# Optimization experiments

Measured on AMD Instinct MI355X. Metric: run time of the kernel, lower is better.

## Reference

```python
import jax, jax.numpy as jnp
import numpy as np

LN_EPS = 1e-9
NEG_INF = float(-2**32 + 1)


def setup_inputs() -> dict:
    key = jax.random.key(0)
    k1, k2 = jax.random.split(key)
    B, T, C = 64, 1024, 256
    x = jax.random.normal(k1, (B, T, C), dtype=jnp.float32)
    key_masks = jax.random.randint(k2, (B, 1, T), 0, 2) > 0  # bool [B,1,T]
    gamma = jnp.ones((C,), dtype=jnp.float32)
    beta = jnp.zeros((C,), dtype=jnp.float32)
    return {"x": x, "key_masks": key_masks, "gamma": gamma, "beta": beta}


def reference(x, key_masks, gamma, beta):
    # x: [B,T,C]; key_masks: [B,1,T] bool; gamma/beta: [C]
    B, T, C = x.shape
    inv_scale = 1.0 / np.sqrt(C).astype(np.float32)
    # DotAttention: QK^T scaled -> [B,T,T]
    align = jnp.einsum('btc,bsc->bts', x, x) * inv_scale
    # key padding mask (broadcast over query axis)
    align = jnp.where(key_masks, align, NEG_INF)
    # future binding: causal lower-triangular mask
    causal = jnp.tril(jnp.ones((T, T), dtype=bool))
    align = jnp.where(causal[None, :, :], align, NEG_INF)
    attn = jax.nn.softmax(align, axis=-1)  # dropout_rate=0 / inference -> identity
    out = jnp.einsum('bts,bsc->btc', attn, x)  # [B,T,C]
    # LayerNorm over last axis
    mu = jnp.mean(out, axis=-1, keepdims=True)
    var = jnp.mean(jnp.square(out - mu), axis=-1, keepdims=True)
    out = gamma * (out - mu) * jax.lax.rsqrt(var + LN_EPS) + beta
    # reduce_mean over time axis, keepdims
    return jnp.mean(out, axis=1, keepdims=True)  # [B,1,C]
```

## Files before the change

kernel.cpp:

```cpp
#include <hip/hip_runtime.h>

#define B_   64
#define T_   1024
#define C_   256
#define NEGF (-4294967295.0f)
#define LN_EPS 1e-9f

typedef short  short8 __attribute__((ext_vector_type(8)));
typedef float  f32x4  __attribute__((ext_vector_type(4)));

union S8 { short8 v; unsigned int w[4]; };

__device__ __forceinline__ unsigned int pk2(float x, float y) {
  unsigned a = __float_as_uint(x); a = (a + 0x7fffu + ((a >> 16) & 1u)) >> 16;
  unsigned b = __float_as_uint(y); b = (b + 0x7fffu + ((b >> 16) & 1u)) >> 16;
  return a | (b << 16);
}

__device__ __forceinline__ void async16(const void* g, void* l) {
  __builtin_amdgcn_global_load_lds(
      (const __attribute__((address_space(1))) void*)g,
      (__attribute__((address_space(3))) void*)l,
      16, 0, 0);
}


__global__ void detect_kernel(const unsigned int* __restrict__ mw,
                              int* __restrict__ flag) {
  int idx = blockIdx.x * 256 + threadIdx.x;
  if (mw[idx] > 1u) atomicOr(flag, 1);
}

__global__ void finalize_kernel(const float* __restrict__ accum,
                                float* __restrict__ out) {
  int idx = blockIdx.x * 256 + threadIdx.x;
  out[idx] = accum[idx] * (1.0f / T_);
}

__global__ __launch_bounds__(256) void convert_kv(const float* __restrict__ x,
                                                  const unsigned int* __restrict__ mw,
                                                  const int* __restrict__ flag,
                                                  short* __restrict__ xk,
                                                  short* __restrict__ xv,
                                                  float* __restrict__ colsum,
                                                  float2* __restrict__ sb) {
  __shared__ float Xt[32 * 256];
  const int blk = blockIdx.x, b = blk >> 5, tt = blk & 31;
  const int tid = threadIdx.x;
  const float* xt = x + (size_t)(b * 1024 + tt * 32) * 256;

  if (tid < 32) {
    int idx = b * 1024 + tt * 32 + tid;
    int f = *flag;
    unsigned int w = mw[f ? (idx >> 2) : idx];
    unsigned int v = f ? ((w >> ((idx & 3) * 8)) & 0xffu) : w;
    sb[idx] = v ? make_float2(0.0625f, 0.f) : make_float2(0.f, NEGF);
  }

#pragma unroll
  for (int u = 0; u < 4; ++u) {
    int id = u * 256 + tid;
    int row = id >> 5, ck = id & 31;
    const float* src = xt + row * 256 + ck * 8;
    float4 a  = *(const float4*)src;
    float4 c4 = *(const float4*)(src + 4);
    *(float4*)&Xt[row * 256 + ck * 8]     = a;
    *(float4*)&Xt[row * 256 + ck * 8 + 4] = c4;
    S8 s; s.w[0] = pk2(a.x, a.y);  s.w[1] = pk2(a.z, a.w);
          s.w[2] = pk2(c4.x, c4.y); s.w[3] = pk2(c4.z, c4.w);
    *(short8*)(xk + (size_t)(b * 1024 + tt * 32 + row) * 256 + ((ck ^ row) << 3)) = s.v;
  }
  __syncthreads();

  const int ck = tid >> 6, clo = tid & 63;
  short* vout = xv + (size_t)(b * 32 + tt) * 8192;
#pragma unroll
  for (int g = 0; g < 4; ++g) {
    int c = g * 64 + clo;
    float vs[8]; float s = 0.f;
#pragma unroll
    for (int e = 0; e < 8; ++e) { vs[e] = Xt[(ck * 8 + e) * 256 + c]; s += vs[e]; }
    S8 o;
    o.w[0] = pk2(vs[0], vs[1]); o.w[1] = pk2(vs[2], vs[3]);
    o.w[2] = pk2(vs[4], vs[5]); o.w[3] = pk2(vs[6], vs[7]);
    *(short8*)(vout + c * 32 + (((ck ^ ((c >> 1) & 3)) & 3) << 3)) = o.v;
    atomicAdd(&colsum[b * 256 + c], s);
  }
}

__device__ __forceinline__ void finalize_tile(
    f32x4* Oa, float m, float l, int b, int quad, int r,
    const float* __restrict__ colsum, const float* __restrict__ gamma,
    const float* __restrict__ beta, float* __restrict__ accum)
{
  float mr[4], li[4];
#pragma unroll
  for (int reg = 0; reg < 4; ++reg) {
    mr[reg] = __shfl(m, quad * 4 + reg, 64);
    float lr = __shfl(l, quad * 4 + reg, 64);
    li[reg] = 1.f / lr;
  }
#pragma unroll
  for (int ct = 0; ct < 16; ++ct) {
    float cs = colsum[b * C_ + ct * 16 + r] * (1.0f / T_);
#pragma unroll
    for (int reg = 0; reg < 4; ++reg)
      Oa[ct][reg] = (mr[reg] < -1.0e9f) ? cs : Oa[ct][reg] * li[reg];
  }
  float ts[16];
#pragma unroll
  for (int ct = 0; ct < 16; ++ct) ts[ct] = 0.f;
#pragma unroll
  for (int reg = 0; reg < 4; ++reg) {
    float s2 = 0.f;
#pragma unroll
    for (int ct = 0; ct < 16; ++ct) s2 += Oa[ct][reg];
    s2 += __shfl_xor(s2, 1, 64); s2 += __shfl_xor(s2, 2, 64);
    s2 += __shfl_xor(s2, 4, 64); s2 += __shfl_xor(s2, 8, 64);
    float mu = s2 * (1.0f / C_);
    float sq = 0.f;
#pragma unroll
    for (int ct = 0; ct < 16; ++ct) { float d = Oa[ct][reg] - mu; sq += d * d; }
    sq += __shfl_xor(sq, 1, 64); sq += __shfl_xor(sq, 2, 64);
    sq += __shfl_xor(sq, 4, 64); sq += __shfl_xor(sq, 8, 64);
    float rstd = rsqrtf(sq * (1.0f / C_) + LN_EPS);
#pragma unroll
    for (int ct = 0; ct < 16; ++ct) {
      int c = ct * 16 + r;
      ts[ct] += gamma[c] * (Oa[ct][reg] - mu) * rstd + beta[c];
    }
  }
#pragma unroll
  for (int ct = 0; ct < 16; ++ct) {
    ts[ct] += __shfl_xor(ts[ct], 16, 64);
    ts[ct] += __shfl_xor(ts[ct], 32, 64);
  }
  if (quad == 0) {
#pragma unroll
    for (int ct = 0; ct < 16; ++ct)
      atomicAdd(&accum[b * C_ + ct * 16 + r], ts[ct]);
  }
}

__global__ __launch_bounds__(512, 2) void flash5(
    const short* __restrict__ xk,
    const short* __restrict__ xv,
    const float2* __restrict__ sb,
    const float* __restrict__ gamma,
    const float* __restrict__ beta,
    const float* __restrict__ colsum,
    float* __restrict__ accum)
{
  __shared__ __align__(16) short KsD[2][64 * 256];
  __shared__ __align__(16) short VtD[2][2 * 256 * 32];

  const int i0 = blockIdx.x;
  const int x8 = i0 & 7;
  const int s  = i0 >> 3;
  const int b  = x8 + 8 * (s & 7);
  const int t  = s >> 3;

  const int tid  = threadIdx.x;
  const int w    = tid >> 6;
  const int lane = tid & 63;
  const int quad = lane >> 4;
  const int r    = lane & 15;

  const int h0len = 2 * (t + 1);

  int qt   = t;
  int n0   = qt * 128 + w * 16;
  int qrow = n0 + r;
  short8 qf[8];
  {
    const short* qp = xk + (size_t)(b * 1024 + qrow) * 256;
#pragma unroll
    for (int ks = 0; ks < 8; ++ks)
      qf[ks] = *(const short8*)(qp + (((ks * 4 + quad) ^ (qrow & 31)) << 3));
  }
  f32x4 Oa[16];
#pragma unroll
  for (int ct = 0; ct < 16; ++ct) Oa[ct] = (f32x4){0.f, 0.f, 0.f, 0.f};
  float m = NEGF, l = 0.f;

  {
    const short* gk = xk + (size_t)(b * 1024) * 256;
    const short* gv = xv + (size_t)(b * 32) * 8192;
#pragma unroll
    for (int u = 0; u < 4; ++u) {
      int seg = w * 4 + u;
      async16(gk + seg * 512 + lane * 8, &KsD[0][seg * 512]);
      async16(gv + seg * 512 + lane * 8, &VtD[0][seg * 512]);
    }
  }
  __syncthreads();

  for (int idx = 0; idx < 18; ++idx) {
    const int ibuf = idx & 1;
    if (idx < 17) {
      const int nt2 = (idx + 1 < h0len) ? (idx + 1) : (17 - (idx + 1));
      const short* gk = xk + (size_t)(b * 1024 + nt2 * 64) * 256;
      const short* gv = xv + (size_t)(b * 32 + nt2 * 2) * 8192;
#pragma unroll
      for (int u = 0; u < 4; ++u) {
        int seg = w * 4 + u;
        async16(gk + seg * 512 + lane * 8, &KsD[1 - ibuf][seg * 512]);
        async16(gv + seg * 512 + lane * 8, &VtD[1 - ibuf][seg * 512]);
      }
    }

    const int kt  = (idx < h0len) ? idx : (17 - idx);
    const int ktb = kt * 64;
    if (ktb <= n0 + 15) {
      float sc[16];
#pragma unroll
      for (int mt = 0; mt < 4; ++mt) {
        f32x4 acc = (f32x4){0.f, 0.f, 0.f, 0.f};
        const int row = mt * 16 + r;
#pragma unroll
        for (int ks = 0; ks < 8; ++ks) {
          short8 af = *(short8*)&KsD[ibuf][row * 256 + (((ks * 4 + quad) ^ (row & 31)) << 3)];
          acc = __builtin_amdgcn_mfma_f32_16x16x32_bf16(af, qf[ks], acc, 0, 0, 0);
        }
        const int j0 = ktb + mt * 16 + quad * 4;
        float4 sA = *(const float4*)(sb + (size_t)b * 1024 + j0);
        float4 sB = *(const float4*)(sb + (size_t)b * 1024 + j0 + 2);
        sc[mt * 4 + 0] = acc[0] * sA.x + sA.y;
        sc[mt * 4 + 1] = acc[1] * sA.z + sA.w;
        sc[mt * 4 + 2] = acc[2] * sB.x + sB.y;
        sc[mt * 4 + 3] = acc[3] * sB.z + sB.w;
      }
      if (ktb + 63 > n0) {
#pragma unroll
        for (int k2 = 0; k2 < 16; ++k2) {
          int j = ktb + (k2 >> 2) * 16 + quad * 4 + (k2 & 3);
          if (j > qrow) sc[k2] = NEGF;
        }
      }

      float mx = sc[0];
#pragma unroll
      for (int k2 = 1; k2 < 16; ++k2) mx = fmaxf(mx, sc[k2]);
      mx = fmaxf(mx, __shfl_xor(mx, 16, 64));
      mx = fmaxf(mx, __shfl_xor(mx, 32, 64));
      float mnew  = fmaxf(m, mx);
      float alpha = __expf(m - mnew);
      float p[16], ps = 0.f;
#pragma unroll
      for (int k2 = 0; k2 < 16; ++k2) { p[k2] = __expf(sc[k2] - mnew); ps += p[k2]; }
      ps += __shfl_xor(ps, 16, 64);
      ps += __shfl_xor(ps, 32, 64);
      l = l * alpha + ps;
      m = mnew;

      if (__ballot(alpha < 1.0f)) {
        float ar[4];
#pragma unroll
        for (int reg = 0; reg < 4; ++reg) ar[reg] = __shfl(alpha, quad * 4 + reg, 64);
#pragma unroll
        for (int ct = 0; ct < 16; ++ct) {
          Oa[ct][0] *= ar[0]; Oa[ct][1] *= ar[1];
          Oa[ct][2] *= ar[2]; Oa[ct][3] *= ar[3];
        }
      }

      S8 pf[2];
#pragma unroll
      for (int hh = 0; hh < 2; ++hh) {
        unsigned q0 = pk2(p[hh * 8 + 0], p[hh * 8 + 1]);
        unsigned q1 = pk2(p[hh * 8 + 2], p[hh * 8 + 3]);
        unsigned q2 = pk2(p[hh * 8 + 4], p[hh * 8 + 5]);
        unsigned q3 = pk2(p[hh * 8 + 6], p[hh * 8 + 7]);
        int s0l = ((quad & 1) << 5) + r, s1l = s0l + 16;
        unsigned u0 = __shfl((int)q0, s0l, 64), u1 = __shfl((int)q1, s0l, 64);
        unsigned u2 = __shfl((int)q2, s0l, 64), u3 = __shfl((int)q3, s0l, 64);
        unsigned v0 = __shfl((int)q0, s1l, 64), v1 = __shfl((int)q1, s1l, 64);
        unsigned v2 = __shfl((int)q2, s1l, 64), v3 = __shfl((int)q3, s1l, 64);
        bool hi = quad >= 2;
        pf[hh].w[0] = hi ? u2 : u0; pf[hh].w[1] = hi ? u3 : u1;
        pf[hh].w[2] = hi ? v2 : v0; pf[hh].w[3] = hi ? v3 : v1;
      }

#pragma unroll
      for (int ct = 0; ct < 16; ++ct) {
        int c = ct * 16 + r;
        int cs_off = c * 32 + (((quad ^ ((c >> 1) & 3)) & 3) << 3);
        short8 b0 = *(short8*)&VtD[ibuf][cs_off];
        short8 b1 = *(short8*)&VtD[ibuf][8192 + cs_off];
        Oa[ct] = __builtin_amdgcn_mfma_f32_16x16x32_bf16(pf[0].v, b0, Oa[ct], 0, 0, 0);
        Oa[ct] = __builtin_amdgcn_mfma_f32_16x16x32_bf16(pf[1].v, b1, Oa[ct], 0, 0, 0);
      }
    }

    if (idx == h0len - 1) {
      finalize_tile(Oa, m, l, b, quad, r, colsum, gamma, beta, accum);
      qt = 7 - t;
      n0 = qt * 128 + w * 16;
      qrow = n0 + r;
      const short* qp = xk + (size_t)(b * 1024 + qrow) * 256;
#pragma unroll
      for (int ks = 0; ks < 8; ++ks)
        qf[ks] = *(const short8*)(qp + (((ks * 4 + quad) ^ (qrow & 31)) << 3));
#pragma unroll
      for (int ct = 0; ct < 16; ++ct) Oa[ct] = (f32x4){0.f, 0.f, 0.f, 0.f};
      m = NEGF; l = 0.f;
    }

    __syncthreads();
  }

  finalize_tile(Oa, m, l, b, quad, r, colsum, gamma, beta, accum);
}


extern "C" void kernel_launch(void* const* d_in, const int* in_sizes, int n_in,
                              void* d_out, int out_size, void* d_ws, size_t ws_size,
                              hipStream_t stream) {
  const float* x     = (const float*)d_in[0];
  const void*  km    = d_in[1];
  const float* gamma = (const float*)d_in[2];
  const float* beta  = (const float*)d_in[3];
  float* out = (float*)d_out;

  const size_t off_sb = 131200;
  const size_t off_xk = 655616;
  const size_t off_xv = off_xk + 33554432;

  float*  accum  = (float*)d_ws;
  float*  colsum = (float*)((char*)d_ws + 65536);
  int*    flag   = (int*)((char*)d_ws + 131072);
  float2* sb     = (float2*)((char*)d_ws + off_sb);
  short*  xk     = (short*)((char*)d_ws + off_xk);
  short*  xv     = (short*)((char*)d_ws + off_xv);

  hipMemsetAsync(d_ws, 0, 131136, stream);
  detect_kernel<<<64, 256, 0, stream>>>((const unsigned int*)km, flag);
  convert_kv<<<B_ * 32, 256, 0, stream>>>(x, (const unsigned int*)km, flag,
                                          xk, xv, colsum, sb);
  flash5<<<256, 512, 0, stream>>>(xk, xv, sb, gamma, beta, colsum, accum);
  finalize_kernel<<<B_ * C_ / 256, 256, 0, stream>>>(accum, out);
}
```

Measured before the change: 181.4 us.

## Restructure flash kernel to 4-wave blocks with two query tiles per wave

```diff
diff --git a/kernel.cpp b/kernel.cpp
--- a/kernel.cpp
+++ b/kernel.cpp
@@ -5,6 +5,7 @@
 #define C_   256
 #define NEGF (-4294967295.0f)
 #define LN_EPS 1e-9f
+#define XTS  260
 
 typedef short  short8 __attribute__((ext_vector_type(8)));
 typedef float  f32x4  __attribute__((ext_vector_type(4)));
@@ -44,10 +45,13 @@
                                                   short* __restrict__ xv,
                                                   float* __restrict__ colsum,
                                                   float2* __restrict__ sb) {
-  __shared__ float Xt[32 * 256];
+  __shared__ float Xt[32 * XTS];
+  __shared__ float csum[256];
   const int blk = blockIdx.x, b = blk >> 5, tt = blk & 31;
   const int tid = threadIdx.x;
   const float* xt = x + (size_t)(b * 1024 + tt * 32) * 256;
+
+  csum[tid] = 0.f;
 
   if (tid < 32) {
     int idx = b * 1024 + tt * 32 + tid;
@@ -64,8 +68,8 @@
     const float* src = xt + row * 256 + ck * 8;
     float4 a  = *(const float4*)src;
     float4 c4 = *(const float4*)(src + 4);
-    *(float4*)&Xt[row * 256 + ck * 8]     = a;
-    *(float4*)&Xt[row * 256 + ck * 8 + 4] = c4;
+    *(float4*)&Xt[row * XTS + ck * 8]     = a;
+    *(float4*)&Xt[row * XTS + ck * 8 + 4] = c4;
     S8 s; s.w[0] = pk2(a.x, a.y);  s.w[1] = pk2(a.z, a.w);
           s.w[2] = pk2(c4.x, c4.y); s.w[3] = pk2(c4.z, c4.w);
     *(short8*)(xk + (size_t)(b * 1024 + tt * 32 + row) * 256 + ((ck ^ row) << 3)) = s.v;
@@ -79,13 +83,56 @@
     int c = g * 64 + clo;
     float vs[8]; float s = 0.f;
 #pragma unroll
-    for (int e = 0; e < 8; ++e) { vs[e] = Xt[(ck * 8 + e) * 256 + c]; s += vs[e]; }
+    for (int e = 0; e < 8; ++e) { vs[e] = Xt[(ck * 8 + e) * XTS + c]; s += vs[e]; }
     S8 o;
     o.w[0] = pk2(vs[0], vs[1]); o.w[1] = pk2(vs[2], vs[3]);
     o.w[2] = pk2(vs[4], vs[5]); o.w[3] = pk2(vs[6], vs[7]);
     *(short8*)(vout + c * 32 + (((ck ^ ((c >> 1) & 3)) & 3) << 3)) = o.v;
-    atomicAdd(&colsum[b * 256 + c], s);
-  }
+    atomicAdd(&csum[c], s);
+  }
+  __syncthreads();
+  atomicAdd(&colsum[b * 256 + tid], csum[tid]);
+}
+
+
+__device__ __forceinline__ S8 softmax_step(const float* sc, float& m, float& l,
+                                           f32x4* Oa, int quad, int r) {
+  float mx = sc[0];
+#pragma unroll
+  for (int k2 = 1; k2 < 8; ++k2) mx = fmaxf(mx, sc[k2]);
+  mx = fmaxf(mx, __shfl_xor(mx, 16, 64));
+  mx = fmaxf(mx, __shfl_xor(mx, 32, 64));
+  float mnew  = fmaxf(m, mx);
+  float alpha = __expf(m - mnew);
+  float p[8], ps = 0.f;
+#pragma unroll
+  for (int k2 = 0; k2 < 8; ++k2) { p[k2] = __expf(sc[k2] - mnew); ps += p[k2]; }
+  ps += __shfl_xor(ps, 16, 64);
+  ps += __shfl_xor(ps, 32, 64);
+  l = l * alpha + ps;
+  m = mnew;
+  if (__ballot(alpha < 1.0f)) {
+    float ar[4];
+#pragma unroll
+    for (int reg = 0; reg < 4; ++reg) ar[reg] = __shfl(alpha, quad * 4 + reg, 64);
+#pragma unroll
+    for (int ct = 0; ct < 16; ++ct) {
+      Oa[ct][0] *= ar[0]; Oa[ct][1] *= ar[1];
+      Oa[ct][2] *= ar[2]; Oa[ct][3] *= ar[3];
+    }
+  }
+  unsigned q0 = pk2(p[0], p[1]), q1 = pk2(p[2], p[3]);
+  unsigned q2 = pk2(p[4], p[5]), q3 = pk2(p[6], p[7]);
+  int s0l = ((quad & 1) << 5) + r, s1l = s0l + 16;
+  unsigned u0 = __shfl((int)q0, s0l, 64), u1 = __shfl((int)q1, s0l, 64);
+  unsigned u2 = __shfl((int)q2, s0l, 64), u3 = __shfl((int)q3, s0l, 64);
+  unsigned v0 = __shfl((int)q0, s1l, 64), v1 = __shfl((int)q1, s1l, 64);
+  unsigned v2 = __shfl((int)q2, s1l, 64), v3 = __shfl((int)q3, s1l, 64);
+  bool hi = quad >= 2;
+  S8 pf;
+  pf.w[0] = hi ? u2 : u0; pf.w[1] = hi ? u3 : u1;
+  pf.w[2] = hi ? v2 : v0; pf.w[3] = hi ? v3 : v1;
+  return pf;
 }
 
 __device__ __forceinline__ void finalize_tile(
@@ -142,7 +189,7 @@
   }
 }
 
-__global__ __launch_bounds__(512, 2) void flash5(
+__global__ __launch_bounds__(256, 2) void flash7(
     const short* __restrict__ xk,
     const short* __restrict__ xv,
     const float2* __restrict__ sb,
@@ -151,14 +198,18 @@
     const float* __restrict__ colsum,
     float* __restrict__ accum)
 {
-  __shared__ __align__(16) short KsD[2][64 * 256];
-  __shared__ __align__(16) short VtD[2][2 * 256 * 32];
-
-  const int i0 = blockIdx.x;
-  const int x8 = i0 & 7;
-  const int s  = i0 >> 3;
-  const int b  = x8 + 8 * (s & 7);
-  const int t  = s >> 3;
+  __shared__ __align__(16) short KsD[2][32 * 256];
+  __shared__ __align__(16) short VtD[2][256 * 32];
+
+  const int i0   = blockIdx.x;
+  const int half = i0 >> 8;
+  const int j    = i0 & 255;
+  const int x8   = j & 7;
+  const int v    = j >> 3;
+  const int b    = x8 + 8 * (v & 7);
+  const int tc   = v >> 3;
+  const int tau  = half ? tc : (7 - tc);
+  const int niters = 4 * tau + 4;
 
   const int tid  = threadIdx.x;
   const int w    = tid >> 6;
@@ -166,22 +217,28 @@
   const int quad = lane >> 4;
   const int r    = lane & 15;
 
-  const int h0len = 2 * (t + 1);
-
-  int qt   = t;
-  int n0   = qt * 128 + w * 16;
-  int qrow = n0 + r;
-  short8 qf[8];
+  const int n0a = tau * 128 + w * 16;
+  const int n0b = n0a + 64;
+  const int qrowA = n0a + r, qrowB = n0b + r;
+
+  short8 qfA[8], qfB[8];
   {
-    const short* qp = xk + (size_t)(b * 1024 + qrow) * 256;
-#pragma unroll
-    for (int ks = 0; ks < 8; ++ks)
-      qf[ks] = *(const short8*)(qp + (((ks * 4 + quad) ^ (qrow & 31)) << 3));
-  }
-  f32x4 Oa[16];
-#pragma unroll
-  for (int ct = 0; ct < 16; ++ct) Oa[ct] = (f32x4){0.f, 0.f, 0.f, 0.f};
-  float m = NEGF, l = 0.f;
+    const short* qa = xk + (size_t)(b * 1024 + qrowA) * 256;
+    const short* qb = xk + (size_t)(b * 1024 + qrowB) * 256;
+#pragma unroll
+    for (int ks = 0; ks < 8; ++ks) {
+      qfA[ks] = *(const short8*)(qa + (((ks * 4 + quad) ^ (qrowA & 31)) << 3));
+      qfB[ks] = *(const short8*)(qb + (((ks * 4 + quad) ^ (qrowB & 31)) << 3));
+    }
+  }
+
+  f32x4 OaA[16], OaB[16];
+#pragma unroll
+  for (int ct = 0; ct < 16; ++ct) {
+    OaA[ct] = (f32x4){0.f, 0.f, 0.f, 0.f};
+    OaB[ct] = (f32x4){0.f, 0.f, 0.f, 0.f};
+  }
+  float mA = NEGF, lA = 0.f, mB = NEGF, lB = 0.f;
 
   {
     const short* gk = xk + (size_t)(b * 1024) * 256;
@@ -195,12 +252,11 @@
   }
   __syncthreads();
 
-  for (int idx = 0; idx < 18; ++idx) {
-    const int ibuf = idx & 1;
-    if (idx < 17) {
-      const int nt2 = (idx + 1 < h0len) ? (idx + 1) : (17 - (idx + 1));
-      const short* gk = xk + (size_t)(b * 1024 + nt2 * 64) * 256;
-      const short* gv = xv + (size_t)(b * 32 + nt2 * 2) * 8192;
+  for (int kt = 0; kt < niters; ++kt) {
+    const int ibuf = kt & 1;
+    if (kt + 1 < niters) {
+      const short* gk = xk + (size_t)(b * 1024 + (kt + 1) * 32) * 256;
+      const short* gv = xv + (size_t)(b * 32 + (kt + 1)) * 8192;
 #pragma unroll
       for (int u = 0; u < 4; ++u) {
         int seg = w * 4 + u;
@@ -209,107 +265,76 @@
       }
     }
 
-    const int kt  = (idx < h0len) ? idx : (17 - idx);
-    const int ktb = kt * 64;
-    if (ktb <= n0 + 15) {
-      float sc[16];
-#pragma unroll
-      for (int mt = 0; mt < 4; ++mt) {
-        f32x4 acc = (f32x4){0.f, 0.f, 0.f, 0.f};
+    const int ktb = kt * 32;
+    const bool bAct = (ktb <= n0b + 15);
+    const bool aAct = (ktb <= n0a + 15);
+    if (bAct) {
+      float scA[8], scB[8];
+#pragma unroll
+      for (int mt = 0; mt < 2; ++mt) {
+        f32x4 aA = (f32x4){0.f, 0.f, 0.f, 0.f};
+        f32x4 aB = (f32x4){0.f, 0.f, 0.f, 0.f};
         const int row = mt * 16 + r;
 #pragma unroll
         for (int ks = 0; ks < 8; ++ks) {
-          short8 af = *(short8*)&KsD[ibuf][row * 256 + (((ks * 4 + quad) ^ (row & 31)) << 3)];
-          acc = __builtin_amdgcn_mfma_f32_16x16x32_bf16(af, qf[ks], acc, 0, 0, 0);
+          short8 af = *(short8*)&KsD[ibuf][row * 256 + (((ks * 4 + quad) ^ row) << 3)];
+          aB = __builtin_amdgcn_mfma_f32_16x16x32_bf16(af, qfB[ks], aB, 0, 0, 0);
+          if (aAct)
+            aA = __builtin_amdgcn_mfma_f32_16x16x32_bf16(af, qfA[ks], aA, 0, 0, 0);
         }
         const int j0 = ktb + mt * 16 + quad * 4;
-        float4 sA = *(const float4*)(sb + (size_t)b * 1024 + j0);
-        float4 sB = *(const float4*)(sb + (size_t)b * 1024 + j0 + 2);
-        sc[mt * 4 + 0] = acc[0] * sA.x + sA.y;
-        sc[mt * 4 + 1] = acc[1] * sA.z + sA.w;
-        sc[mt * 4 + 2] = acc[2] * sB.x + sB.y;
-        sc[mt * 4 + 3] = acc[3] * sB.z + sB.w;
-      }
-      if (ktb + 63 > n0) {
-#pragma unroll
-        for (int k2 = 0; k2 < 16; ++k2) {
-          int j = ktb + (k2 >> 2) * 16 + quad * 4 + (k2 & 3);
-          if (j > qrow) sc[k2] = NEGF;
-        }
-      }
-
-      float mx = sc[0];
-#pragma unroll
-      for (int k2 = 1; k2 < 16; ++k2) mx = fmaxf(mx, sc[k2]);
-      mx = fmaxf(mx, __shfl_xor(mx, 16, 64));
-      mx = fmaxf(mx, __shfl_xor(mx, 32, 64));
-      float mnew  = fmaxf(m, mx);
-      float alpha = __expf(m - mnew);
-      float p[16], ps = 0.f;
-#pragma unroll
-      for (int k2 = 0; k2 < 16; ++k2) { p[k2] = __expf(sc[k2] - mnew); ps += p[k2]; }
-      ps += __shfl_xor(ps, 16, 64);
-      ps += __shfl_xor(ps, 32, 64);
-      l = l * alpha + ps;
-      m = mnew;
-
-      if (__ballot(alpha < 1.0f)) {
-        float ar[4];
-#pragma unroll
-        for (int reg = 0; reg < 4; ++reg) ar[reg] = __shfl(alpha, quad * 4 + reg, 64);
+        float4 s4a = *(const float4*)(sb + (size_t)b * 1024 + j0);
+        float4 s4b = *(const float4*)(sb + (size_t)b * 1024 + j0 + 2);
+        scB[mt * 4 + 0] = aB[0] * s4a.x + s4a.y;
+        scB[mt * 4 + 1] = aB[1] * s4a.z + s4a.w;
+        scB[mt * 4 + 2] = aB[2] * s4b.x + s4b.y;
+        scB[mt * 4 + 3] = aB[3] * s4b.z + s4b.w;
+        if (aAct) {
+          scA[mt * 4 + 0] = aA[0] * s4a.x + s4a.y;
+          scA[mt * 4 + 1] = aA[1] * s4a.z + s4a.w;
+          scA[mt * 4 + 2] = aA[2] * s4b.x + s4b.y;
+          scA[mt * 4 + 3] = aA[3] * s4b.z + s4b.w;
+        }
+      }
+      if (ktb + 31 > n0b) {
+#pragma unroll
+        for (int k2 = 0; k2 < 8; ++k2) {
+          int jj = ktb + (k2 >> 2) * 16 + quad * 4 + (k2 & 3);
+          if (jj > qrowB) scB[k2] = NEGF;
+        }
+      }
+      if (aAct && ktb + 31 > n0a) {
+#pragma unroll
+        for (int k2 = 0; k2 < 8; ++k2) {
+          int jj = ktb + (k2 >> 2) * 16 + quad * 4 + (k2 & 3);
+          if (jj > qrowA) scA[k2] = NEGF;
+        }
+      }
+
+      S8 pfB = softmax_step(scB, mB, lB, OaB, quad, r);
+      if (aAct) {
+        S8 pfA = softmax_step(scA, mA, lA, OaA, quad, r);
 #pragma unroll
         for (int ct = 0; ct < 16; ++ct) {
-          Oa[ct][0] *= ar[0]; Oa[ct][1] *= ar[1];
-          Oa[ct][2] *= ar[2]; Oa[ct][3] *= ar[3];
-        }
-      }
-
-      S8 pf[2];
-#pragma unroll
-      for (int hh = 0; hh < 2; ++hh) {
-        unsigned q0 = pk2(p[hh * 8 + 0], p[hh * 8 + 1]);
-        unsigned q1 = pk2(p[hh * 8 + 2], p[hh * 8 + 3]);
-        unsigned q2 = pk2(p[hh * 8 + 4], p[hh * 8 + 5]);
-        unsigned q3 = pk2(p[hh * 8 + 6], p[hh * 8 + 7]);
-        int s0l = ((quad & 1) << 5) + r, s1l = s0l + 16;
-        unsigned u0 = __shfl((int)q0, s0l, 64), u1 = __shfl((int)q1, s0l, 64);
-        unsigned u2 = __shfl((int)q2, s0l, 64), u3 = __shfl((int)q3, s0l, 64);
-        unsigned v0 = __shfl((int)q0, s1l, 64), v1 = __shfl((int)q1, s1l, 64);
-        unsigned v2 = __shfl((int)q2, s1l, 64), v3 = __shfl((int)q3, s1l, 64);
-        bool hi = quad >= 2;
-        pf[hh].w[0] = hi ? u2 : u0; pf[hh].w[1] = hi ? u3 : u1;
-        pf[hh].w[2] = hi ? v2 : v0; pf[hh].w[3] = hi ? v3 : v1;
-      }
-
-#pragma unroll
-      for (int ct = 0; ct < 16; ++ct) {
-        int c = ct * 16 + r;
-        int cs_off = c * 32 + (((quad ^ ((c >> 1) & 3)) & 3) << 3);
-        short8 b0 = *(short8*)&VtD[ibuf][cs_off];
-        short8 b1 = *(short8*)&VtD[ibuf][8192 + cs_off];
-        Oa[ct] = __builtin_amdgcn_mfma_f32_16x16x32_bf16(pf[0].v, b0, Oa[ct], 0, 0, 0);
-        Oa[ct] = __builtin_amdgcn_mfma_f32_16x16x32_bf16(pf[1].v, b1, Oa[ct], 0, 0, 0);
-      }
-    }
-
-    if (idx == h0len - 1) {
-      finalize_tile(Oa, m, l, b, quad, r, colsum, gamma, beta, accum);
-      qt = 7 - t;
-      n0 = qt * 128 + w * 16;
-      qrow = n0 + r;
-      const short* qp = xk + (size_t)(b * 1024 + qrow) * 256;
-#pragma unroll
-      for (int ks = 0; ks < 8; ++ks)
-        qf[ks] = *(const short8*)(qp + (((ks * 4 + quad) ^ (qrow & 31)) << 3));
-#pragma unroll
-      for (int ct = 0; ct < 16; ++ct) Oa[ct] = (f32x4){0.f, 0.f, 0.f, 0.f};
-      m = NEGF; l = 0.f;
-    }
-
+          int c = ct * 16 + r;
+          short8 bf = *(short8*)&VtD[ibuf][c * 32 + (((quad ^ ((c >> 1) & 3)) & 3) << 3)];
+          OaB[ct] = __builtin_amdgcn_mfma_f32_16x16x32_bf16(pfB.v, bf, OaB[ct], 0, 0, 0);
+          OaA[ct] = __builtin_amdgcn_mfma_f32_16x16x32_bf16(pfA.v, bf, OaA[ct], 0, 0, 0);
+        }
+      } else {
+#pragma unroll
+        for (int ct = 0; ct < 16; ++ct) {
+          int c = ct * 16 + r;
+          short8 bf = *(short8*)&VtD[ibuf][c * 32 + (((quad ^ ((c >> 1) & 3)) & 3) << 3)];
+          OaB[ct] = __builtin_amdgcn_mfma_f32_16x16x32_bf16(pfB.v, bf, OaB[ct], 0, 0, 0);
+        }
+      }
+    }
     __syncthreads();
   }
 
-  finalize_tile(Oa, m, l, b, quad, r, colsum, gamma, beta, accum);
+  finalize_tile(OaA, mA, lA, b, quad, r, colsum, gamma, beta, accum);
+  finalize_tile(OaB, mB, lB, b, quad, r, colsum, gamma, beta, accum);
 }
 
 
@@ -337,6 +362,6 @@
   detect_kernel<<<64, 256, 0, stream>>>((const unsigned int*)km, flag);
   convert_kv<<<B_ * 32, 256, 0, stream>>>(x, (const unsigned int*)km, flag,
                                           xk, xv, colsum, sb);
-  flash5<<<256, 512, 0, stream>>>(xk, xv, sb, gamma, beta, colsum, accum);
+  flash7<<<512, 256, 0, stream>>>(xk, xv, sb, gamma, beta, colsum, accum);
   finalize_kernel<<<B_ * C_ / 256, 256, 0, stream>>>(accum, out);
 }
```

Result: slower. 394.3 us (+117.3%).
